# Performance work log

Hardware: AMD Instinct MI355X
Metric: run time of the kernel (lower is better)

Reference implementation:

```python
import jax, jax.numpy as jnp
import numpy as np

V = 30522   # vocab / node count
A = 2       # num adjacency matrices
H = 128     # hid_dim
O = 16      # out_dim
B = 8       # batch
D = 256     # doc/sequence dim
NNZ = 250000  # nonzeros per adjacency


def setup_inputs() -> dict:
    key = jax.random.key(0)
    k = jax.random.split(key, 7)
    x_dv = jax.random.normal(k[0], (B, D, V), jnp.float32)
    adj_rows = jax.random.randint(k[1], (A, NNZ), 0, V)
    adj_cols = jax.random.randint(k[2], (A, NNZ), 0, V)
    adj_vals = jax.random.uniform(k[3], (A, NNZ), jnp.float32)
    W_vh = jax.random.normal(k[4], (A, V, H), jnp.float32) * 0.02
    fc_W = jax.random.normal(k[5], (H, O), jnp.float32) * 0.05
    fc_b = jnp.zeros((O,), jnp.float32)
    return {"x_dv": x_dv, "adj_rows": adj_rows, "adj_cols": adj_cols,
            "adj_vals": adj_vals, "W_vh": W_vh, "fc_W": fc_W, "fc_b": fc_b}


def reference(x_dv, adj_rows, adj_cols, adj_vals, W_vh, fc_W, fc_b):
    # Per-adjacency sparse mm: h_vh[a] = A_a @ W_a, A_a in COO form. [A, V, H]
    def spmm(rows, cols, vals, W):
        # gather rows of W at cols, scale by vals, scatter-add into output rows
        return jax.ops.segment_sum(vals[:, None] * W[cols], rows, num_segments=V)

    h_vh = jax.vmap(spmm)(adj_rows, adj_cols, adj_vals, W_vh)  # [A, V, H]
    # Dropout is identity in eval mode. fused_h = sum_a x_dv @ h_vh[a]
    # = x_dv @ sum_a h_vh[a] (x_dv is shared across adjacencies).
    h_sum = h_vh.sum(axis=0)                                   # [V, H]
    fused_h = jnp.einsum('bdv,vh->bdh', x_dv, h_sum)           # [B, D, H]
    return fused_h @ fc_W + fc_b                               # [B, D, O]
```

## Files before the change

### kernel.cpp

```cpp
#include <hip/hip_runtime.h>

#define V_N 30522
#define A_N 2
#define H_N 128
#define O_N 16
#define NNZ_N 250000
#define NNZ_T (A_N * NNZ_N)
#define M_N 2048
#define AV_N (A_N * V_N)

#define KPAD 30720
#define KSPL 32
#define KC (KPAD / KSPL)
#define NCHUNK 30

typedef __attribute__((ext_vector_type(8))) short bf16x8_t;
typedef __attribute__((ext_vector_type(4))) float f32x4_t;

static __device__ __forceinline__ unsigned short f2bf(float f) {
    union { float f; unsigned u; } v; v.f = f;
    unsigned r = v.u + 0x7fffu + ((v.u >> 16) & 1u);
    return (unsigned short)(r >> 16);
}

__global__ __launch_bounds__(256) void wfc_kernel(const float* __restrict__ W,
                                                  const float* __restrict__ fcW,
                                                  float* __restrict__ wfc) {
    __shared__ float wrow[16][128];
    int row0 = blockIdx.x * 16;
    for (int idx = threadIdx.x; idx < 16 * 32; idx += 256) {
        int r = idx >> 5, c4 = (idx & 31) * 4;
        int grow = row0 + r;
        float4 v = make_float4(0.f, 0.f, 0.f, 0.f);
        if (grow < AV_N)
            v = *reinterpret_cast<const float4*>(W + (size_t)grow * H_N + c4);
        *reinterpret_cast<float4*>(&wrow[r][c4]) = v;
    }
    __syncthreads();
    int r = threadIdx.x >> 4, o = threadIdx.x & 15;
    int grow = row0 + r;
    if (grow >= AV_N) return;
    float s = 0.f;
#pragma unroll
    for (int h = 0; h < H_N; ++h) s += wrow[r][h] * fcW[h * O_N + o];
    wfc[(size_t)grow * O_N + o] = s;
}

__global__ __launch_bounds__(256) void hist_kernel(const int* __restrict__ rows,
                                                   int* __restrict__ count) {
    int n = blockIdx.x * blockDim.x + threadIdx.x;
    if (n >= NNZ_T) return;
    atomicAdd(&count[rows[n]], 1);
}

__global__ __launch_bounds__(1024) void scanA_kernel(const int* __restrict__ count,
                                                     int* __restrict__ csum) {
    __shared__ int sdata[1024];
    int tid = threadIdx.x;
    int i = blockIdx.x * 1024 + tid;
    sdata[tid] = (i < V_N) ? count[i] : 0;
    __syncthreads();
    for (int off = 512; off > 0; off >>= 1) {
        if (tid < off) sdata[tid] += sdata[tid + off];
        __syncthreads();
    }
    if (tid == 0) csum[blockIdx.x] = sdata[0];
}

__global__ void scanB_kernel(const int* __restrict__ csum,
                             int* __restrict__ coff,
                             int* __restrict__ row_start) {
    if (threadIdx.x == 0 && blockIdx.x == 0) {
        int run = 0;
        for (int b = 0; b < NCHUNK; ++b) { coff[b] = run; run += csum[b]; }
        row_start[V_N] = run;
    }
}

__global__ __launch_bounds__(1024) void scanC_kernel(const int* __restrict__ count,
                                                     const int* __restrict__ coff,
                                                     int* __restrict__ row_start,
                                                     int* __restrict__ cursor) {
    __shared__ int sdata[1024];
    int tid = threadIdx.x;
    int i = blockIdx.x * 1024 + tid;
    int v = (i < V_N) ? count[i] : 0;
    sdata[tid] = v;
    __syncthreads();
    for (int off = 1; off < 1024; off <<= 1) {
        int t = (tid >= off) ? sdata[tid - off] : 0;
        __syncthreads();
        sdata[tid] += t;
        __syncthreads();
    }
    int exc = sdata[tid] - v + coff[blockIdx.x];
    if (i < V_N) { row_start[i] = exc; cursor[i] = exc; }
}

__global__ __launch_bounds__(256) void scatter_kernel(const int* __restrict__ rows,
                                                      const int* __restrict__ cols,
                                                      const float* __restrict__ vals,
                                                      int* __restrict__ cursor,
                                                      unsigned long long* __restrict__ scv) {
    int n = blockIdx.x * blockDim.x + threadIdx.x;
    if (n >= NNZ_T) return;
    int a = n / NNZ_N;
    int r = rows[n];
    int pos = atomicAdd(&cursor[r], 1);
    union { float f; unsigned u; } uv; uv.f = vals[n];
    scv[pos] = ((unsigned long long)uv.u << 32) | (unsigned)(a * V_N + cols[n]);
}

__global__ __launch_bounds__(256) void accum_hw_kernel(const int* __restrict__ row_start,
                                                       const unsigned long long* __restrict__ scv,
                                                       const float* __restrict__ wfc,
                                                       short* __restrict__ hw_t) {
    int gid = blockIdx.x * blockDim.x + threadIdx.x;
    if (gid >= V_N * O_N) return;
    int row = gid >> 4, o = gid & 15;
    int s = row_start[row];
    int e = row_start[row + 1];
    float acc = 0.f;
    for (int i = s; i < e; ++i) {
        unsigned long long cv = scv[i];
        int cp = (int)(cv & 0xffffffffu);
        union { unsigned u; float f; } uv; uv.u = (unsigned)(cv >> 32);
        acc += uv.f * wfc[(size_t)cp * O_N + o];
    }
    hw_t[(size_t)o * KPAD + row] = (short)f2bf(acc);
}

__global__ __launch_bounds__(256) void init_out_kernel(const float* __restrict__ fcb,
                                                       float* __restrict__ out) {
    int idx = blockIdx.x * blockDim.x + threadIdx.x;
    if (idx >= M_N * O_N) return;
    out[idx] = fcb[idx & 15];
}

__global__ __launch_bounds__(256) void gemm_mfma4(const float* __restrict__ X,
                                                  const short* __restrict__ hw_t,
                                                  float* __restrict__ out) {
    const int tid = threadIdx.x;
    const int w = tid >> 6;
    const int lane = tid & 63;
    const int l15 = lane & 15;
    const int kg = lane >> 4;
    const int row0 = blockIdx.x * 64 + w * 16;
    const int k0 = blockIdx.y * KC;

    const float* xrow = X + (size_t)(row0 + l15) * V_N;
    const short* hrow = hw_t + (size_t)l15 * KPAD;

    f32x4_t acc = {};

#pragma unroll 2
    for (int kb = k0; kb < k0 + KC; kb += 32) {
        int k = kb + kg * 8;
        float a[8];
        if (k + 7 < V_N) {
            const float2* p = reinterpret_cast<const float2*>(xrow + k);
            float2 u0 = p[0], u1 = p[1], u2 = p[2], u3 = p[3];
            a[0] = u0.x; a[1] = u0.y; a[2] = u1.x; a[3] = u1.y;
            a[4] = u2.x; a[5] = u2.y; a[6] = u3.x; a[7] = u3.y;
        } else {
#pragma unroll
            for (int j = 0; j < 8; ++j) a[j] = (k + j < V_N) ? xrow[k + j] : 0.f;
        }
        bf16x8_t av;
#pragma unroll
        for (int j = 0; j < 8; ++j) av[j] = (short)f2bf(a[j]);
        bf16x8_t bv = *reinterpret_cast<const bf16x8_t*>(hrow + k);
        acc = __builtin_amdgcn_mfma_f32_16x16x32_bf16(av, bv, acc, 0, 0, 0);
    }

#pragma unroll
    for (int r4 = 0; r4 < 4; ++r4)
        atomicAdd(&out[(size_t)(row0 + kg * 4 + r4) * O_N + l15], acc[r4]);
}

extern "C" void kernel_launch(void* const* d_in, const int* in_sizes, int n_in,
                              void* d_out, int out_size, void* d_ws, size_t ws_size,
                              hipStream_t stream) {
    const float* x    = (const float*)d_in[0];
    const int* rows   = (const int*)d_in[1];
    const int* cols   = (const int*)d_in[2];
    const float* vals = (const float*)d_in[3];
    const float* W    = (const float*)d_in[4];
    const float* fcW  = (const float*)d_in[5];
    const float* fcb  = (const float*)d_in[6];
    float* out = (float*)d_out;

    char* base = (char*)d_ws;
    size_t off = 0;
    auto alloc = [&](size_t bytes) { size_t p = off; off = (off + bytes + 255) & ~(size_t)255; return p; };
    size_t o_wfc    = alloc((size_t)AV_N * O_N * 4);
    size_t o_hwt    = alloc((size_t)O_N * KPAD * 2);
    size_t o_count  = alloc((size_t)V_N * 4);
    size_t o_rstart = alloc((size_t)(V_N + 1) * 4);
    size_t o_cursor = alloc((size_t)V_N * 4);
    size_t o_scv    = alloc((size_t)NNZ_T * 8);
    size_t o_csum   = alloc((size_t)NCHUNK * 4);
    size_t o_coff   = alloc((size_t)NCHUNK * 4);

    float* wfc        = (float*)(base + o_wfc);
    short* hw_t       = (short*)(base + o_hwt);
    int*   count      = (int*)(base + o_count);
    int*   row_start  = (int*)(base + o_rstart);
    int*   cursor     = (int*)(base + o_cursor);
    unsigned long long* scv = (unsigned long long*)(base + o_scv);
    int*   csum       = (int*)(base + o_csum);
    int*   coff       = (int*)(base + o_coff);

    hipMemsetAsync(count, 0, (size_t)V_N * 4, stream);
    hipMemsetAsync(hw_t, 0, (size_t)O_N * KPAD * 2, stream);

    wfc_kernel<<<(AV_N + 15) / 16, 256, 0, stream>>>(W, fcW, wfc);
    hist_kernel<<<(NNZ_T + 255) / 256, 256, 0, stream>>>(rows, count);
    scanA_kernel<<<NCHUNK, 1024, 0, stream>>>(count, csum);
    scanB_kernel<<<1, 64, 0, stream>>>(csum, coff, row_start);
    scanC_kernel<<<NCHUNK, 1024, 0, stream>>>(count, coff, row_start, cursor);
    scatter_kernel<<<(NNZ_T + 255) / 256, 256, 0, stream>>>(rows, cols, vals, cursor, scv);
    accum_hw_kernel<<<(V_N * O_N + 255) / 256, 256, 0, stream>>>(row_start, scv, wfc, hw_t);

    init_out_kernel<<<(M_N * O_N + 255) / 256, 256, 0, stream>>>(fcb, out);
    gemm_mfma4<<<dim3(M_N / 64, KSPL), 256, 0, stream>>>(x, hw_t, out);
}
```

Before: 177.6 us.

## Fuse all stages into one persistent cooperative kernel with grid syncs

```diff
diff --git a/kernel.cpp b/kernel.cpp
--- a/kernel.cpp
+++ b/kernel.cpp
@@ -1,4 +1,7 @@
 #include <hip/hip_runtime.h>
+#include <hip/hip_cooperative_groups.h>
+
+namespace cg = cooperative_groups;
 
 #define V_N 30522
 #define A_N 2
@@ -12,7 +15,8 @@
 #define KPAD 30720
 #define KSPL 32
 #define KC (KPAD / KSPL)
-#define NCHUNK 30
+#define TOTB 1024
+#define NCH 120
 
 typedef __attribute__((ext_vector_type(8))) short bf16x8_t;
 typedef __attribute__((ext_vector_type(4))) float f32x4_t;
@@ -23,159 +27,172 @@
     return (unsigned short)(r >> 16);
 }
 
-__global__ __launch_bounds__(256) void wfc_kernel(const float* __restrict__ W,
-                                                  const float* __restrict__ fcW,
-                                                  float* __restrict__ wfc) {
+__global__ __launch_bounds__(256, 4) void fused_all(
+    int phase, int nblk,
+    const float* __restrict__ X, const int* __restrict__ rows,
+    const int* __restrict__ cols, const float* __restrict__ vals,
+    const float* __restrict__ W, const float* __restrict__ fcW,
+    const float* __restrict__ fcb, float* __restrict__ out,
+    float* __restrict__ wfc, short* __restrict__ hw_t,
+    int* __restrict__ count, int* __restrict__ row_start,
+    int* __restrict__ cursor, unsigned long long* __restrict__ scv,
+    int* __restrict__ csum) {
+    cg::grid_group grid = cg::this_grid();
+    const bool coop = (phase < 0);
+    const int tid = threadIdx.x;
+    const int bid = blockIdx.x;
+    const int gt = nblk * 256;
+    const int gtid = bid * 256 + tid;
+
     __shared__ float wrow[16][128];
-    int row0 = blockIdx.x * 16;
-    for (int idx = threadIdx.x; idx < 16 * 32; idx += 256) {
-        int r = idx >> 5, c4 = (idx & 31) * 4;
-        int grow = row0 + r;
-        float4 v = make_float4(0.f, 0.f, 0.f, 0.f);
-        if (grow < AV_N)
-            v = *reinterpret_cast<const float4*>(W + (size_t)grow * H_N + c4);
-        *reinterpret_cast<float4*>(&wrow[r][c4]) = v;
-    }
-    __syncthreads();
-    int r = threadIdx.x >> 4, o = threadIdx.x & 15;
-    int grow = row0 + r;
-    if (grow >= AV_N) return;
-    float s = 0.f;
-#pragma unroll
-    for (int h = 0; h < H_N; ++h) s += wrow[r][h] * fcW[h * O_N + o];
-    wfc[(size_t)grow * O_N + o] = s;
-}
-
-__global__ __launch_bounds__(256) void hist_kernel(const int* __restrict__ rows,
-                                                   int* __restrict__ count) {
-    int n = blockIdx.x * blockDim.x + threadIdx.x;
-    if (n >= NNZ_T) return;
-    atomicAdd(&count[rows[n]], 1);
-}
-
-__global__ __launch_bounds__(1024) void scanA_kernel(const int* __restrict__ count,
-                                                     int* __restrict__ csum) {
-    __shared__ int sdata[1024];
-    int tid = threadIdx.x;
-    int i = blockIdx.x * 1024 + tid;
-    sdata[tid] = (i < V_N) ? count[i] : 0;
-    __syncthreads();
-    for (int off = 512; off > 0; off >>= 1) {
-        if (tid < off) sdata[tid] += sdata[tid + off];
-        __syncthreads();
-    }
-    if (tid == 0) csum[blockIdx.x] = sdata[0];
-}
-
-__global__ void scanB_kernel(const int* __restrict__ csum,
-                             int* __restrict__ coff,
-                             int* __restrict__ row_start) {
-    if (threadIdx.x == 0 && blockIdx.x == 0) {
-        int run = 0;
-        for (int b = 0; b < NCHUNK; ++b) { coff[b] = run; run += csum[b]; }
-        row_start[V_N] = run;
-    }
-}
-
-__global__ __launch_bounds__(1024) void scanC_kernel(const int* __restrict__ count,
-                                                     const int* __restrict__ coff,
-                                                     int* __restrict__ row_start,
-                                                     int* __restrict__ cursor) {
-    __shared__ int sdata[1024];
-    int tid = threadIdx.x;
-    int i = blockIdx.x * 1024 + tid;
-    int v = (i < V_N) ? count[i] : 0;
-    sdata[tid] = v;
-    __syncthreads();
-    for (int off = 1; off < 1024; off <<= 1) {
-        int t = (tid >= off) ? sdata[tid - off] : 0;
-        __syncthreads();
-        sdata[tid] += t;
-        __syncthreads();
-    }
-    int exc = sdata[tid] - v + coff[blockIdx.x];
-    if (i < V_N) { row_start[i] = exc; cursor[i] = exc; }
-}
-
-__global__ __launch_bounds__(256) void scatter_kernel(const int* __restrict__ rows,
-                                                      const int* __restrict__ cols,
-                                                      const float* __restrict__ vals,
-                                                      int* __restrict__ cursor,
-                                                      unsigned long long* __restrict__ scv) {
-    int n = blockIdx.x * blockDim.x + threadIdx.x;
-    if (n >= NNZ_T) return;
-    int a = n / NNZ_N;
-    int r = rows[n];
-    int pos = atomicAdd(&cursor[r], 1);
-    union { float f; unsigned u; } uv; uv.f = vals[n];
-    scv[pos] = ((unsigned long long)uv.u << 32) | (unsigned)(a * V_N + cols[n]);
-}
-
-__global__ __launch_bounds__(256) void accum_hw_kernel(const int* __restrict__ row_start,
-                                                       const unsigned long long* __restrict__ scv,
-                                                       const float* __restrict__ wfc,
-                                                       short* __restrict__ hw_t) {
-    int gid = blockIdx.x * blockDim.x + threadIdx.x;
-    if (gid >= V_N * O_N) return;
-    int row = gid >> 4, o = gid & 15;
-    int s = row_start[row];
-    int e = row_start[row + 1];
-    float acc = 0.f;
-    for (int i = s; i < e; ++i) {
-        unsigned long long cv = scv[i];
-        int cp = (int)(cv & 0xffffffffu);
-        union { unsigned u; float f; } uv; uv.u = (unsigned)(cv >> 32);
-        acc += uv.f * wfc[(size_t)cp * O_N + o];
-    }
-    hw_t[(size_t)o * KPAD + row] = (short)f2bf(acc);
-}
-
-__global__ __launch_bounds__(256) void init_out_kernel(const float* __restrict__ fcb,
-                                                       float* __restrict__ out) {
-    int idx = blockIdx.x * blockDim.x + threadIdx.x;
-    if (idx >= M_N * O_N) return;
-    out[idx] = fcb[idx & 15];
-}
-
-__global__ __launch_bounds__(256) void gemm_mfma4(const float* __restrict__ X,
-                                                  const short* __restrict__ hw_t,
-                                                  float* __restrict__ out) {
-    const int tid = threadIdx.x;
-    const int w = tid >> 6;
-    const int lane = tid & 63;
-    const int l15 = lane & 15;
-    const int kg = lane >> 4;
-    const int row0 = blockIdx.x * 64 + w * 16;
-    const int k0 = blockIdx.y * KC;
-
-    const float* xrow = X + (size_t)(row0 + l15) * V_N;
-    const short* hrow = hw_t + (size_t)l15 * KPAD;
-
-    f32x4_t acc = {};
+    __shared__ int sdata[256];
+    __shared__ int base_s;
+
+    if (coop || phase == 0) {
+        if (gtid < M_N * O_N) out[gtid] = fcb[gtid & 15];
+        if (gtid < V_N) count[gtid] = 0;
+        {
+            const int padw = KPAD - V_N;
+            for (int idx = gtid; idx < O_N * padw; idx += gt) {
+                int o = idx / padw, v2 = V_N + (idx - o * padw);
+                hw_t[(size_t)o * KPAD + v2] = 0;
+            }
+        }
+        for (int t = bid; t < (AV_N + 15) / 16; t += nblk) {
+            int row0 = t * 16;
+            for (int idx = tid; idx < 16 * 32; idx += 256) {
+                int r = idx >> 5, c4 = (idx & 31) * 4;
+                int grow = row0 + r;
+                float4 v = make_float4(0.f, 0.f, 0.f, 0.f);
+                if (grow < AV_N)
+                    v = *reinterpret_cast<const float4*>(W + (size_t)grow * H_N + c4);
+                *reinterpret_cast<float4*>(&wrow[r][c4]) = v;
+            }
+            __syncthreads();
+            int r = tid >> 4, o = tid & 15;
+            int grow = row0 + r;
+            if (grow < AV_N) {
+                float s = 0.f;
+#pragma unroll
+                for (int h = 0; h < H_N; ++h) s += wrow[r][h] * fcW[h * O_N + o];
+                wfc[(size_t)grow * O_N + o] = s;
+            }
+            __syncthreads();
+        }
+    }
+    if (coop) grid.sync();
+
+    if (coop || phase == 1) {
+        for (int n = gtid; n < NNZ_T; n += gt) atomicAdd(&count[rows[n]], 1);
+    }
+    if (coop) grid.sync();
+
+    if (coop || phase == 2) {
+        if (bid < NCH) {
+            int i = bid * 256 + tid;
+            int v = (i < V_N) ? count[i] : 0;
+            sdata[tid] = v;
+            __syncthreads();
+            for (int off2 = 1; off2 < 256; off2 <<= 1) {
+                int t2 = (tid >= off2) ? sdata[tid - off2] : 0;
+                __syncthreads();
+                sdata[tid] += t2;
+                __syncthreads();
+            }
+            if (i < V_N) row_start[i] = sdata[tid] - v;
+            if (tid == 255) csum[bid] = sdata[255];
+        }
+    }
+    if (coop) grid.sync();
+
+    if (coop || phase == 3) {
+        if (bid < NCH) {
+            if (tid == 0) {
+                int s = 0;
+                for (int j = 0; j < bid; ++j) s += csum[j];
+                base_s = s;
+                if (bid == NCH - 1) row_start[V_N] = s + csum[NCH - 1];
+            }
+            __syncthreads();
+            int i = bid * 256 + tid;
+            if (i < V_N) {
+                int rs = row_start[i] + base_s;
+                row_start[i] = rs;
+                cursor[i] = rs;
+            }
+        }
+    }
+    if (coop) grid.sync();
+
+    if (coop || phase == 4) {
+        for (int n = gtid; n < NNZ_T; n += gt) {
+            int a = n / NNZ_N;
+            int r = rows[n];
+            int pos = atomicAdd(&cursor[r], 1);
+            union { float f; unsigned u; } uv; uv.f = vals[n];
+            scv[pos] = ((unsigned long long)uv.u << 32) | (unsigned)(a * V_N + cols[n]);
+        }
+    }
+    if (coop) grid.sync();
+
+    if (coop || phase == 5) {
+        for (int g = gtid; g < V_N * O_N; g += gt) {
+            int row = g >> 4, o = g & 15;
+            int s = row_start[row];
+            int e = row_start[row + 1];
+            float acc = 0.f;
+            for (int i = s; i < e; ++i) {
+                unsigned long long cv = scv[i];
+                int cp = (int)(cv & 0xffffffffu);
+                union { unsigned u; float f; } uv; uv.u = (unsigned)(cv >> 32);
+                acc += uv.f * wfc[(size_t)cp * O_N + o];
+            }
+            hw_t[(size_t)o * KPAD + row] = (short)f2bf(acc);
+        }
+    }
+    if (coop) grid.sync();
+
+    if (coop || phase == 6) {
+        const int w = tid >> 6;
+        const int lane = tid & 63;
+        const int l15 = lane & 15;
+        const int kg = lane >> 4;
+        for (int t6 = bid; t6 < TOTB; t6 += nblk) {
+            const int bx = t6 & 31;
+            const int by = t6 >> 5;
+            const int row0g = bx * 64 + w * 16;
+            const int k0 = by * KC;
+
+            const float* xrow = X + (size_t)(row0g + l15) * V_N;
+            const short* hrow = hw_t + (size_t)l15 * KPAD;
+
+            f32x4_t acc = {};
 
 #pragma unroll 2
-    for (int kb = k0; kb < k0 + KC; kb += 32) {
-        int k = kb + kg * 8;
-        float a[8];
-        if (k + 7 < V_N) {
-            const float2* p = reinterpret_cast<const float2*>(xrow + k);
-            float2 u0 = p[0], u1 = p[1], u2 = p[2], u3 = p[3];
-            a[0] = u0.x; a[1] = u0.y; a[2] = u1.x; a[3] = u1.y;
-            a[4] = u2.x; a[5] = u2.y; a[6] = u3.x; a[7] = u3.y;
-        } else {
-#pragma unroll
-            for (int j = 0; j < 8; ++j) a[j] = (k + j < V_N) ? xrow[k + j] : 0.f;
-        }
-        bf16x8_t av;
-#pragma unroll
-        for (int j = 0; j < 8; ++j) av[j] = (short)f2bf(a[j]);
-        bf16x8_t bv = *reinterpret_cast<const bf16x8_t*>(hrow + k);
-        acc = __builtin_amdgcn_mfma_f32_16x16x32_bf16(av, bv, acc, 0, 0, 0);
-    }
-
-#pragma unroll
-    for (int r4 = 0; r4 < 4; ++r4)
-        atomicAdd(&out[(size_t)(row0 + kg * 4 + r4) * O_N + l15], acc[r4]);
+            for (int kb = k0; kb < k0 + KC; kb += 32) {
+                int k = kb + kg * 8;
+                float a[8];
+                if (k + 7 < V_N) {
+                    const float2* p = reinterpret_cast<const float2*>(xrow + k);
+                    float2 u0 = p[0], u1 = p[1], u2 = p[2], u3 = p[3];
+                    a[0] = u0.x; a[1] = u0.y; a[2] = u1.x; a[3] = u1.y;
+                    a[4] = u2.x; a[5] = u2.y; a[6] = u3.x; a[7] = u3.y;
+                } else {
+#pragma unroll
+                    for (int j = 0; j < 8; ++j) a[j] = (k + j < V_N) ? xrow[k + j] : 0.f;
+                }
+                bf16x8_t av;
+#pragma unroll
+                for (int j = 0; j < 8; ++j) av[j] = (short)f2bf(a[j]);
+                bf16x8_t bv = *reinterpret_cast<const bf16x8_t*>(hrow + k);
+                acc = __builtin_amdgcn_mfma_f32_16x16x32_bf16(av, bv, acc, 0, 0, 0);
+            }
+
+#pragma unroll
+            for (int r4 = 0; r4 < 4; ++r4)
+                atomicAdd(&out[(size_t)(row0g + kg * 4 + r4) * O_N + l15], acc[r4]);
+        }
+    }
 }
 
 extern "C" void kernel_launch(void* const* d_in, const int* in_sizes, int n_in,
@@ -199,8 +216,7 @@
     size_t o_rstart = alloc((size_t)(V_N + 1) * 4);
     size_t o_cursor = alloc((size_t)V_N * 4);
     size_t o_scv    = alloc((size_t)NNZ_T * 8);
-    size_t o_csum   = alloc((size_t)NCHUNK * 4);
-    size_t o_coff   = alloc((size_t)NCHUNK * 4);
+    size_t o_csum   = alloc((size_t)NCH * 4);
 
     float* wfc        = (float*)(base + o_wfc);
     short* hw_t       = (short*)(base + o_hwt);
@@ -209,19 +225,41 @@
     int*   cursor     = (int*)(base + o_cursor);
     unsigned long long* scv = (unsigned long long*)(base + o_scv);
     int*   csum       = (int*)(base + o_csum);
-    int*   coff       = (int*)(base + o_coff);
-
-    hipMemsetAsync(count, 0, (size_t)V_N * 4, stream);
-    hipMemsetAsync(hw_t, 0, (size_t)O_N * KPAD * 2, stream);
-
-    wfc_kernel<<<(AV_N + 15) / 16, 256, 0, stream>>>(W, fcW, wfc);
-    hist_kernel<<<(NNZ_T + 255) / 256, 256, 0, stream>>>(rows, count);
-    scanA_kernel<<<NCHUNK, 1024, 0, stream>>>(count, csum);
-    scanB_kernel<<<1, 64, 0, stream>>>(csum, coff, row_start);
-    scanC_kernel<<<NCHUNK, 1024, 0, stream>>>(count, coff, row_start, cursor);
-    scatter_kernel<<<(NNZ_T + 255) / 256, 256, 0, stream>>>(rows, cols, vals, cursor, scv);
-    accum_hw_kernel<<<(V_N * O_N + 255) / 256, 256, 0, stream>>>(row_start, scv, wfc, hw_t);
-
-    init_out_kernel<<<(M_N * O_N + 255) / 256, 256, 0, stream>>>(fcb, out);
-    gemm_mfma4<<<dim3(M_N / 64, KSPL), 256, 0, stream>>>(x, hw_t, out);
+
+    int dev = 0;
+    (void)hipGetDevice(&dev);
+    int ncu = 0;
+    {
+        hipDeviceProp_t props;
+        if (hipGetDeviceProperties(&props, dev) == hipSuccess)
+            ncu = props.multiProcessorCount;
+    }
+    int maxBlk = 0;
+    hipError_t qerr = hipOccupancyMaxActiveBlocksPerMultiprocessor(
+        &maxBlk, (const void*)fused_all, 256, 0);
+    int nblk = 0;
+    if (qerr == hipSuccess && maxBlk > 0 && ncu > 0) {
+        long long cap = (long long)maxBlk * ncu;
+        nblk = (cap < TOTB) ? (int)cap : TOTB;
+    }
+
+    bool done = false;
+    if (nblk >= NCH) {
+        int phase = -1;
+        void* kargs[] = {
+            (void*)&phase, (void*)&nblk,
+            (void*)&x, (void*)&rows, (void*)&cols, (void*)&vals,
+            (void*)&W, (void*)&fcW, (void*)&fcb, (void*)&out,
+            (void*)&wfc, (void*)&hw_t, (void*)&count, (void*)&row_start,
+            (void*)&cursor, (void*)&scv, (void*)&csum,
+        };
+        done = (hipLaunchCooperativeKernel((const void*)fused_all, dim3(nblk),
+                                           dim3(256), kargs, 0, stream) == hipSuccess);
+    }
+    if (!done) {
+        for (int p = 0; p <= 6; ++p)
+            fused_all<<<TOTB, 256, 0, stream>>>(p, TOTB, x, rows, cols, vals, W, fcW,
+                                                fcb, out, wfc, hw_t, count, row_start,
+                                                cursor, scv, csum);
+    }
 }
```

New measurement: 608.4 us. 243% more time.

## Replace split-K atomics with partial buffer reduction and fold memsets into kernels

Applied to the files above, without the earlier changes.

```diff
diff --git a/kernel.cpp b/kernel.cpp
--- a/kernel.cpp
+++ b/kernel.cpp
@@ -13,6 +13,7 @@
 #define KSPL 32
 #define KC (KPAD / KSPL)
 #define NCHUNK 30
+#define PADW (KPAD - V_N)
 
 typedef __attribute__((ext_vector_type(8))) short bf16x8_t;
 typedef __attribute__((ext_vector_type(4))) float f32x4_t;
@@ -25,7 +26,11 @@
 
 __global__ __launch_bounds__(256) void wfc_kernel(const float* __restrict__ W,
                                                   const float* __restrict__ fcW,
-                                                  float* __restrict__ wfc) {
+                                                  float* __restrict__ wfc,
+                                                  int* __restrict__ count) {
+    int gtid = blockIdx.x * 256 + threadIdx.x;
+    if (gtid < V_N) count[gtid] = 0;
+
     __shared__ float wrow[16][128];
     int row0 = blockIdx.x * 16;
     for (int idx = threadIdx.x; idx < 16 * 32; idx += 256) {
@@ -47,8 +52,13 @@
 }
 
 __global__ __launch_bounds__(256) void hist_kernel(const int* __restrict__ rows,
-                                                   int* __restrict__ count) {
+                                                   int* __restrict__ count,
+                                                   short* __restrict__ hw_t) {
     int n = blockIdx.x * blockDim.x + threadIdx.x;
+    if (n < O_N * PADW) {
+        int o = n / PADW, v2 = V_N + (n - o * PADW);
+        hw_t[(size_t)o * KPAD + v2] = 0;
+    }
     if (n >= NNZ_T) return;
     atomicAdd(&count[rows[n]], 1);
 }
@@ -104,7 +114,7 @@
                                                       unsigned long long* __restrict__ scv) {
     int n = blockIdx.x * blockDim.x + threadIdx.x;
     if (n >= NNZ_T) return;
-    int a = n / NNZ_N;
+    int a = (n >= NNZ_N) ? 1 : 0;
     int r = rows[n];
     int pos = atomicAdd(&cursor[r], 1);
     union { float f; unsigned u; } uv; uv.f = vals[n];
@@ -130,23 +140,17 @@
     hw_t[(size_t)o * KPAD + row] = (short)f2bf(acc);
 }
 
-__global__ __launch_bounds__(256) void init_out_kernel(const float* __restrict__ fcb,
-                                                       float* __restrict__ out) {
-    int idx = blockIdx.x * blockDim.x + threadIdx.x;
-    if (idx >= M_N * O_N) return;
-    out[idx] = fcb[idx & 15];
-}
-
-__global__ __launch_bounds__(256) void gemm_mfma4(const float* __restrict__ X,
+__global__ __launch_bounds__(256) void gemm_mfma5(const float* __restrict__ X,
                                                   const short* __restrict__ hw_t,
-                                                  float* __restrict__ out) {
+                                                  float* __restrict__ partials) {
     const int tid = threadIdx.x;
     const int w = tid >> 6;
     const int lane = tid & 63;
     const int l15 = lane & 15;
     const int kg = lane >> 4;
     const int row0 = blockIdx.x * 64 + w * 16;
-    const int k0 = blockIdx.y * KC;
+    const int by = blockIdx.y;
+    const int k0 = by * KC;
 
     const float* xrow = X + (size_t)(row0 + l15) * V_N;
     const short* hrow = hw_t + (size_t)l15 * KPAD;
@@ -175,7 +179,19 @@
 
 #pragma unroll
     for (int r4 = 0; r4 < 4; ++r4)
-        atomicAdd(&out[(size_t)(row0 + kg * 4 + r4) * O_N + l15], acc[r4]);
+        partials[((size_t)by * M_N + row0 + kg * 4 + r4) * O_N + l15] = acc[r4];
+}
+
+__global__ __launch_bounds__(256) void reduce_kernel(const float* __restrict__ partials,
+                                                     const float* __restrict__ fcb,
+                                                     float* __restrict__ out) {
+    int idx = blockIdx.x * 256 + threadIdx.x;
+    if (idx >= M_N * O_N) return;
+    float s = fcb[idx & 15];
+#pragma unroll
+    for (int by = 0; by < KSPL; ++by)
+        s += partials[(size_t)by * M_N * O_N + idx];
+    out[idx] = s;
 }
 
 extern "C" void kernel_launch(void* const* d_in, const int* in_sizes, int n_in,
@@ -201,6 +217,7 @@
     size_t o_scv    = alloc((size_t)NNZ_T * 8);
     size_t o_csum   = alloc((size_t)NCHUNK * 4);
     size_t o_coff   = alloc((size_t)NCHUNK * 4);
+    size_t o_part   = alloc((size_t)KSPL * M_N * O_N * 4);
 
     float* wfc        = (float*)(base + o_wfc);
     short* hw_t       = (short*)(base + o_hwt);
@@ -210,18 +227,16 @@
     unsigned long long* scv = (unsigned long long*)(base + o_scv);
     int*   csum       = (int*)(base + o_csum);
     int*   coff       = (int*)(base + o_coff);
-
-    hipMemsetAsync(count, 0, (size_t)V_N * 4, stream);
-    hipMemsetAsync(hw_t, 0, (size_t)O_N * KPAD * 2, stream);
-
-    wfc_kernel<<<(AV_N + 15) / 16, 256, 0, stream>>>(W, fcW, wfc);
-    hist_kernel<<<(NNZ_T + 255) / 256, 256, 0, stream>>>(rows, count);
+    float* partials   = (float*)(base + o_part);
+
+    wfc_kernel<<<(AV_N + 15) / 16, 256, 0, stream>>>(W, fcW, wfc, count);
+    hist_kernel<<<(NNZ_T + 255) / 256, 256, 0, stream>>>(rows, count, hw_t);
     scanA_kernel<<<NCHUNK, 1024, 0, stream>>>(count, csum);
     scanB_kernel<<<1, 64, 0, stream>>>(csum, coff, row_start);
     scanC_kernel<<<NCHUNK, 1024, 0, stream>>>(count, coff, row_start, cursor);
     scatter_kernel<<<(NNZ_T + 255) / 256, 256, 0, stream>>>(rows, cols, vals, cursor, scv);
     accum_hw_kernel<<<(V_N * O_N + 255) / 256, 256, 0, stream>>>(row_start, scv, wfc, hw_t);
 
-    init_out_kernel<<<(M_N * O_N + 255) / 256, 256, 0, stream>>>(fcb, out);
-    gemm_mfma4<<<dim3(M_N / 64, KSPL), 256, 0, stream>>>(x, hw_t, out);
-}
+    gemm_mfma5<<<dim3(M_N / 64, KSPL), 256, 0, stream>>>(x, hw_t, partials);
+    reduce_kernel<<<(M_N * O_N + 255) / 256, 256, 0, stream>>>(partials, fcb, out);
+}
```

Measured after the change: 165.9 us. -6.6%, faster.
